# Optimization experiments

Hardware: AMD Instinct MI355X
Metric: run time of the kernel (lower is better)

The kernel has to match this reference:

```python
import jax, jax.numpy as jnp
import numpy as np

NUM_HEADS = 4
KEY_DIMS = 32  # c // num_heads


def rel_to_abs(x):
    # x: [B, N, W, 2W-1] relative logits -> [B, N, W, W] absolute logits
    b, n, w, _ = x.shape
    x = jnp.pad(x, ((0, 0), (0, 0), (0, 0), (0, 1)))           # [b,n,w,2w]
    x = x.reshape(b, n, w * 2 * w)
    x = jnp.pad(x, ((0, 0), (0, 0), (0, w - 1)))
    x = x.reshape(b, n, w + 1, 2 * w - 1)
    return x[:, :, :w, w - 1:]


def rel_logits_1d(q, rel_k):
    # q: [B, heads, X, Y, d], rel_k: [2Y-1, d] -> [B, heads, X, X, Y, Y]
    b, nh, xx, yy, d = q.shape
    rl = jnp.einsum('bhxyd,md->bhxym', q, rel_k)               # [b,h,x,y,2y-1]
    rl = rel_to_abs(rl.reshape(b, nh * xx, yy, 2 * yy - 1))    # [b,h*x,y,y]
    rl = rl.reshape(b, nh, xx, 1, yy, yy)
    return jnp.broadcast_to(rl, (b, nh, xx, xx, yy, yy))


def relative_position_bias(pos_q, pos_emb_h, pos_emb_w):
    # pos_q: [B, heads, H, W, d] -> bias [B, heads, H, W, H, W]
    rw = rel_logits_1d(pos_q, pos_emb_w)                        # [b,h,H,H,W,W]
    rw = rw.transpose(0, 1, 2, 4, 3, 5)                         # [b,h,H,W,H,W]
    rh = rel_logits_1d(pos_q.transpose(0, 1, 3, 2, 4), pos_emb_h)  # [b,h,W,W,H,H]
    rh = rh.transpose(0, 1, 4, 2, 5, 3)                         # [b,h,H,W,H,W]
    return rw + rh


def setup_inputs() -> dict:
    key = jax.random.key(0)
    k1, k2, k3, k4 = jax.random.split(key, 4)
    B, H, W, C = 2, 64, 64, 128
    qk_dims = NUM_HEADS * KEY_DIMS  # 128
    out_channels = C
    x = jax.random.normal(k1, (B, H, W, C), dtype=jnp.float32)
    w_qkv = jax.random.normal(k2, (C, 2 * qk_dims + out_channels), dtype=jnp.float32) * 0.05
    pos_emb_h = jax.random.normal(k3, (2 * H - 1, KEY_DIMS), dtype=jnp.float32) * 0.05
    pos_emb_w = jax.random.normal(k4, (2 * W - 1, KEY_DIMS), dtype=jnp.float32) * 0.05
    return {'x': x, 'w_qkv': w_qkv, 'pos_emb_h': pos_emb_h, 'pos_emb_w': pos_emb_w}


def reference(x, w_qkv, pos_emb_h, pos_emb_w):
    B, H, W, C = x.shape
    nh, kd = NUM_HEADS, KEY_DIMS
    qk_dims = nh * kd
    oc = C
    scale = 1.0 / float(kd) ** 0.5

    qkv = jnp.einsum('bhwc,cd->bhwd', x, w_qkv)                 # 1x1 conv, no bias
    q, k, v = jnp.split(qkv, [qk_dims, 2 * qk_dims], axis=-1)
    L = H * W
    q = q.reshape(B, L, nh, kd).transpose(0, 2, 1, 3)           # [B,nh,L,kd]
    k = k.reshape(B, L, nh, kd).transpose(0, 2, 1, 3)           # [B,nh,L,kd]
    v = v.reshape(B, L, nh, oc // nh).transpose(0, 2, 1, 3)     # [B,nh,L,dv]

    pos_q = q.reshape(B, nh, H, W, kd)
    pos = relative_position_bias(pos_q, pos_emb_h, pos_emb_w).reshape(B, nh, L, L)

    scores = jnp.einsum('bnqd,bnkd->bnqk', q, k) * scale + pos  # [B,nh,L,L]
    attn = jax.nn.softmax(scores, axis=-1)
    out = jnp.einsum('bnqk,bnkd->bnqd', attn, v)                # [B,nh,L,dv]
    out = out.transpose(0, 2, 1, 3).reshape(B, H, W, oc)
    return out
```

## Files before the change

### kernel.cpp

```cpp
#include <hip/hip_runtime.h>
#include <hip/hip_bf16.h>
#include <math.h>

#define B_  2
#define NH  4
#define HH  64
#define WW  64
#define KD  32
#define L_  4096
#define BN_ 8
#define LOG2E 1.4426950408889634f
#define KSCALE (0.17677669529663687f * 1.4426950408889634f)
#define FIXED_M 10.0f

typedef float    f32x4  __attribute__((ext_vector_type(4), may_alias));
typedef _Float16 half8  __attribute__((ext_vector_type(8), may_alias));
typedef _Float16 half4  __attribute__((ext_vector_type(4), may_alias));
typedef __fp16   fp16x2 __attribute__((ext_vector_type(2)));
typedef unsigned uint4v __attribute__((ext_vector_type(4)));

__device__ __forceinline__ float fexp2(float x) {
#if __has_builtin(__builtin_amdgcn_exp2f)
    return __builtin_amdgcn_exp2f(x);
#else
    return __expf(x * 0.69314718056f);
#endif
}

__device__ __forceinline__ unsigned pack2u(float a, float b) {
    fp16x2 t = __builtin_amdgcn_cvt_pkrtz(a, b);
    union { fp16x2 i; unsigned o; } u;
    u.i = t;
    return u.o;
}

__global__ __launch_bounds__(256) void qkv_gemm(const float* __restrict__ x,
                                                const float* __restrict__ w,
                                                _Float16* __restrict__ q_h,
                                                _Float16* __restrict__ k_h,
                                                _Float16* __restrict__ vt_h) {
    __shared__ __align__(16) char smem[34816];
    _Float16* xs  = (_Float16*)smem;
    _Float16* wsT = (_Float16*)(smem + 17408);

    const int mt = blockIdx.x % 128;
    const int nt = blockIdx.x / 128;
    const int m0 = mt * 64, n0 = nt * 64;
    const int tid = threadIdx.x;
    const int wv = tid >> 6, lane = tid & 63;
    const int l16 = lane & 15, quad = lane >> 4;

    #pragma unroll
    for (int i = 0; i < 8; i++) {
        const int idx = i * 256 + tid;
        const int row = idx >> 5, c4 = (idx & 31) * 4;
        const float4 v = *(const float4*)&x[(size_t)(m0 + row) * 128 + c4];
        half4 h;
        h[0] = (_Float16)v.x; h[1] = (_Float16)v.y;
        h[2] = (_Float16)v.z; h[3] = (_Float16)v.w;
        *(half4*)&xs[row * 136 + c4] = h;
    }
    #pragma unroll
    for (int i = 0; i < 8; i++) {
        const int idx = i * 256 + tid;
        const int k = idx >> 4, c4 = (idx & 15) * 4;
        const float4 v = *(const float4*)&w[(size_t)k * 384 + n0 + c4];
        wsT[(c4 + 0) * 136 + k] = (_Float16)v.x;
        wsT[(c4 + 1) * 136 + k] = (_Float16)v.y;
        wsT[(c4 + 2) * 136 + k] = (_Float16)v.z;
        wsT[(c4 + 3) * 136 + k] = (_Float16)v.w;
    }
    __syncthreads();

    f32x4 acc[4] = {{0.f,0.f,0.f,0.f},{0.f,0.f,0.f,0.f},
                    {0.f,0.f,0.f,0.f},{0.f,0.f,0.f,0.f}};
    half8 af[4];
    #pragma unroll
    for (int kc = 0; kc < 4; kc++)
        af[kc] = *(const half8*)&xs[(wv * 16 + l16) * 136 + kc * 32 + quad * 8];
    #pragma unroll
    for (int ns = 0; ns < 4; ns++)
        #pragma unroll
        for (int kc = 0; kc < 4; kc++) {
            const half8 bf = *(const half8*)&wsT[(ns * 16 + l16) * 136 + kc * 32 + quad * 8];
            acc[ns] = __builtin_amdgcn_mfma_f32_16x16x32_f16(af[kc], bf, acc[ns], 0, 0, 0);
        }

    const int which = n0 >> 7;
    const int nc = n0 & 127;
    const int b = m0 >> 12;
    if (which < 2) {
        _Float16* dst = (which == 0) ? q_h : k_h;
        const float mult = (which == 1) ? KSCALE : 1.0f;
        #pragma unroll
        for (int ns = 0; ns < 4; ns++) {
            const int col = nc + ns * 16 + l16;
            const int bn = b * NH + (col >> 5);
            const int d = col & 31;
            #pragma unroll
            for (int r = 0; r < 4; r++) {
                const int l = (m0 & 4095) + wv * 16 + quad * 4 + r;
                dst[((size_t)bn * L_ + l) * 32 + d] = (_Float16)(acc[ns][r] * mult);
            }
        }
    } else {
        __syncthreads();
        float* img = (float*)smem;
        #pragma unroll
        for (int ns = 0; ns < 4; ns++) {
            const int chan = ns * 16 + l16;
            const int h = chan >> 5, d = chan & 31;
            #pragma unroll
            for (int r = 0; r < 4; r++) {
                const int p = wv * 16 + quad * 4 + r;
                const int y = p >> 5, p32 = p & 31;
                const int q4 = (p32 >> 2) & 3;
                const int j = ((p32 >> 4) & 1) * 4 + (p32 & 3);
                const int fidx = h * 2048 + (y * 2 + (d >> 4)) * 512
                               + (q4 * 16 + (d & 15)) * 8 + j;
                img[fidx + (fidx >> 4)] = acc[ns][r];
            }
        }
        __syncthreads();
        const int ktg = (m0 & 4095) >> 6;
        #pragma unroll
        for (int h = 0; h < 2; h++) {
            const int head = (nc >> 5) + h;
            const int bn = b * NH + head;
            const int fbase = h * 2048 + tid * 8;
            const int sbase = fbase + (fbase >> 4);
            half8 o;
            #pragma unroll
            for (int e = 0; e < 8; e++) o[e] = (_Float16)img[sbase + e];
            *(half8*)(vt_h + (size_t)bn * 131072 + ktg * 2048 + tid * 8) = o;
        }
    }
}

__global__ __launch_bounds__(512, 4) void attn_mfma(
    const _Float16* __restrict__ q_h,
    const _Float16* __restrict__ k_h,
    const _Float16* __restrict__ vt_h,
    const float* __restrict__ emb_h,
    const float* __restrict__ emb_w,
    float* __restrict__ out)
{
    __shared__ __align__(16) char smem[33792];

    const int bi   = blockIdx.x;
    const int bn   = bi & 7;
    const int w1   = bi >> 3;
    const int tid  = threadIdx.x;
    const int wv   = tid >> 6;
    const int qwv  = wv & 3;
    const int kh   = wv >> 2;
    const int lane = tid & 63;
    const int l16  = lane & 15;
    const int quad = lane >> 4;
    const int q0   = qwv * 16;

    float* Rl = (float*)smem;

    const half8 aq = *(const half8*)(q_h +
        (((size_t)bn * L_ + (q0 + l16) * 64 + w1) * 32 + quad * 8));

    const _Float16* Kbase = k_h  + (size_t)bn * L_ * 32;
    const _Float16* Vtile = vt_h + (size_t)bn * 131072;
    const int lo = lane * 8;
    const int kt0 = kh * 32;
    const int phase = ((wv & 3) << 3) | ((wv >> 2) << 2);

    int kt = kt0 + phase;
    half8 kf[4];
    #pragma unroll
    for (int sub = 0; sub < 4; sub++)
        kf[sub] = *(const half8*)(Kbase + (size_t)(kt * 64 + sub * 16 + l16) * 32 + quad * 8);

    f32x4 qwT[4];
    #pragma unroll
    for (int sub = 0; sub < 4; sub++) {
        const float* ew = emb_w + (size_t)(sub * 16 + l16 - w1 + 63) * 32 + quad * 8;
        const float4 e0 = *(const float4*)ew;
        const float4 e1 = *(const float4*)(ew + 4);
        union { uint4v u; half8 h; } ua;
        ua.u[0] = pack2u(e0.x * LOG2E, e0.y * LOG2E);
        ua.u[1] = pack2u(e0.z * LOG2E, e0.w * LOG2E);
        ua.u[2] = pack2u(e1.x * LOG2E, e1.y * LOG2E);
        ua.u[3] = pack2u(e1.z * LOG2E, e1.w * LOG2E);
        f32x4 z = {-FIXED_M, -FIXED_M, -FIXED_M, -FIXED_M};
        qwT[sub] = __builtin_amdgcn_mfma_f32_16x16x32_f16(ua.h, aq, z, 0, 0, 0);
    }

    #pragma unroll
    for (int ji = 0; ji < 4; ji++) {
        const int jt = kh * 4 + ji;
        int j = jt * 16 + l16; if (j > 126) j = 126;
        const float* eh = emb_h + (size_t)j * 32 + quad * 8;
        const float4 e0 = *(const float4*)eh;
        const float4 e1 = *(const float4*)(eh + 4);
        union { uint4v u; half8 h; } ub;
        ub.u[0] = pack2u(e0.x * LOG2E, e0.y * LOG2E);
        ub.u[1] = pack2u(e0.z * LOG2E, e0.w * LOG2E);
        ub.u[2] = pack2u(e1.x * LOG2E, e1.y * LOG2E);
        ub.u[3] = pack2u(e1.z * LOG2E, e1.w * LOG2E);
        f32x4 z = {0.f, 0.f, 0.f, 0.f};
        const f32x4 C = __builtin_amdgcn_mfma_f32_16x16x32_f16(aq, ub.h, z, 0, 0, 0);
        #pragma unroll
        for (int r = 0; r < 4; r++)
            Rl[(q0 + quad * 4 + r) * 132 + jt * 16 + l16] = C[r];
    }
    __syncthreads();

    f32x4 O0 = {0.f, 0.f, 0.f, 0.f}, O1 = {0.f, 0.f, 0.f, 0.f};
    float l0 = 0.f, l1 = 0.f;
    const float* qh_ptr = Rl + (q0 + l16) * 132 + 63 - (q0 + l16);
#if __has_builtin(__builtin_amdgcn_fdot2)
    fp16x2 onep;
    { union { unsigned u; fp16x2 h; } uo; uo.u = pack2u(1.0f, 1.0f); onep = uo.h; }
#endif

    #pragma unroll 4
    for (int i = 0; i < 32; i++) {
        const _Float16* tb = Vtile + kt * 2048;
        const half8 va00 = *(const half8*)(tb + lo);
        const half8 va10 = *(const half8*)(tb + 512 + lo);
        const half8 va01 = *(const half8*)(tb + 1024 + lo);
        const half8 va11 = *(const half8*)(tb + 1536 + lo);

        const f32x4 S0 = __builtin_amdgcn_mfma_f32_16x16x32_f16(kf[0], aq, qwT[0], 0, 0, 0);
        const f32x4 S1 = __builtin_amdgcn_mfma_f32_16x16x32_f16(kf[1], aq, qwT[1], 0, 0, 0);
        const f32x4 S2 = __builtin_amdgcn_mfma_f32_16x16x32_f16(kf[2], aq, qwT[2], 0, 0, 0);
        const f32x4 S3 = __builtin_amdgcn_mfma_f32_16x16x32_f16(kf[3], aq, qwT[3], 0, 0, 0);

        const float qh_cur = qh_ptr[kt];

        const int ktn = kt0 + (((kt - kt0) + 1) & 31);
        #pragma unroll
        for (int sub = 0; sub < 4; sub++)
            kf[sub] = *(const half8*)(Kbase + (size_t)(ktn * 64 + sub * 16 + l16) * 32 + quad * 8);

        union { uint4v u; half8 h; } pb0, pb1;
        {
            const float a0 = fexp2(S0[0] + qh_cur), a1 = fexp2(S0[1] + qh_cur);
            const float a2 = fexp2(S0[2] + qh_cur), a3 = fexp2(S0[3] + qh_cur);
            const float b0 = fexp2(S1[0] + qh_cur), b1 = fexp2(S1[1] + qh_cur);
            const float b2 = fexp2(S1[2] + qh_cur), b3 = fexp2(S1[3] + qh_cur);
            pb0.u[0] = pack2u(a0, a1); pb0.u[1] = pack2u(a2, a3);
            pb0.u[2] = pack2u(b0, b1); pb0.u[3] = pack2u(b2, b3);
#if __has_builtin(__builtin_amdgcn_fdot2)
            union { unsigned u; fp16x2 h; } c0, c1, c2, c3;
            c0.u = pb0.u[0]; c1.u = pb0.u[1]; c2.u = pb0.u[2]; c3.u = pb0.u[3];
            l0 = __builtin_amdgcn_fdot2(c0.h, onep, l0, false);
            l0 = __builtin_amdgcn_fdot2(c1.h, onep, l0, false);
            l0 = __builtin_amdgcn_fdot2(c2.h, onep, l0, false);
            l0 = __builtin_amdgcn_fdot2(c3.h, onep, l0, false);
#else
            l0 += ((a0 + a1) + (a2 + a3)) + ((b0 + b1) + (b2 + b3));
#endif
        }
        {
            const float a0 = fexp2(S2[0] + qh_cur), a1 = fexp2(S2[1] + qh_cur);
            const float a2 = fexp2(S2[2] + qh_cur), a3 = fexp2(S2[3] + qh_cur);
            const float b0 = fexp2(S3[0] + qh_cur), b1 = fexp2(S3[1] + qh_cur);
            const float b2 = fexp2(S3[2] + qh_cur), b3 = fexp2(S3[3] + qh_cur);
            pb1.u[0] = pack2u(a0, a1); pb1.u[1] = pack2u(a2, a3);
            pb1.u[2] = pack2u(b0, b1); pb1.u[3] = pack2u(b2, b3);
#if __has_builtin(__builtin_amdgcn_fdot2)
            union { unsigned u; fp16x2 h; } c0, c1, c2, c3;
            c0.u = pb1.u[0]; c1.u = pb1.u[1]; c2.u = pb1.u[2]; c3.u = pb1.u[3];
            l1 = __builtin_amdgcn_fdot2(c0.h, onep, l1, false);
            l1 = __builtin_amdgcn_fdot2(c1.h, onep, l1, false);
            l1 = __builtin_amdgcn_fdot2(c2.h, onep, l1, false);
            l1 = __builtin_amdgcn_fdot2(c3.h, onep, l1, false);
#else
            l1 += ((a0 + a1) + (a2 + a3)) + ((b0 + b1) + (b2 + b3));
#endif
        }

        O0 = __builtin_amdgcn_mfma_f32_16x16x32_f16(va00, pb0.h, O0, 0, 0, 0);
        O0 = __builtin_amdgcn_mfma_f32_16x16x32_f16(va01, pb1.h, O0, 0, 0, 0);
        O1 = __builtin_amdgcn_mfma_f32_16x16x32_f16(va10, pb0.h, O1, 0, 0, 0);
        O1 = __builtin_amdgcn_mfma_f32_16x16x32_f16(va11, pb1.h, O1, 0, 0, 0);

        kt = ktn;
    }

    float l = l0 + l1;
    l += __shfl_xor(l, 16);
    l += __shfl_xor(l, 32);

    __syncthreads();
    float (*mO)[32][17] = (float(*)[32][17])smem;
    float* mL = (float*)(smem + 17408);
    #pragma unroll
    for (int r = 0; r < 4; r++) {
        mO[wv][quad * 4 + r][l16]      = O0[r];
        mO[wv][16 + quad * 4 + r][l16] = O1[r];
    }
    if (quad == 0) mL[wv * 16 + l16] = l;
    __syncthreads();

    const int q  = tid >> 3;
    const int dg = tid & 7;
    const int qg = q >> 4, ql = q & 15;
    const float denom = mL[qg * 16 + ql] + mL[(qg + 4) * 16 + ql];
    const float inv = 1.0f / denom;
    float4 o;
    o.x = (mO[qg][dg * 4 + 0][ql] + mO[qg + 4][dg * 4 + 0][ql]) * inv;
    o.y = (mO[qg][dg * 4 + 1][ql] + mO[qg + 4][dg * 4 + 1][ql]) * inv;
    o.z = (mO[qg][dg * 4 + 2][ql] + mO[qg + 4][dg * 4 + 2][ql]) * inv;
    o.w = (mO[qg][dg * 4 + 3][ql] + mO[qg + 4][dg * 4 + 3][ql]) * inv;
    const int head = bn & 3, bb = bn >> 2;
    *(float4*)&out[(((size_t)bb * 64 + q) * 64 + w1) * 128 + head * 32 + dg * 4] = o;
}

extern "C" void kernel_launch(void* const* d_in, const int* in_sizes, int n_in,
                              void* d_out, int out_size, void* d_ws, size_t ws_size,
                              hipStream_t stream) {
    const float* x     = (const float*)d_in[0];
    const float* w_qkv = (const float*)d_in[1];
    const float* emb_h = (const float*)d_in[2];
    const float* emb_w = (const float*)d_in[3];
    float* out = (float*)d_out;

    _Float16* q_h  = (_Float16*)d_ws;
    _Float16* k_h  = q_h + (size_t)BN_ * L_ * KD;
    _Float16* vt_h = k_h + (size_t)BN_ * L_ * KD;

    qkv_gemm<<<768, 256, 0, stream>>>(x, w_qkv, q_h, k_h, vt_h);
    attn_mfma<<<512, 512, 0, stream>>>(q_h, k_h, vt_h, emb_h, emb_w, out);
}
```

Baseline: 122.9 us.

## Prepack QKV weights into MFMA fragment layout and halve GEMM shared memory

Adds a small pre-kernel that converts the weight matrix to fp16 once, folds in the K scale, and lays it out directly in MFMA B-fragment order. The GEMM then loads its weight fragments straight into registers instead of doing a transposed shared-memory staging pass. The V transpose now goes through shared memory one head at a time so the buffer can shrink to 17 KB, at the cost of extra barriers. The attention kernel's per-wave key-tile phase offset is also changed. Together these aim to cut shared-memory traffic and raise occupancy in the projection GEMM, in exchange for an extra launch.

```diff
diff --git a/kernel.cpp b/kernel.cpp
--- a/kernel.cpp
+++ b/kernel.cpp
@@ -34,14 +34,30 @@
     return u.o;
 }
 
+__global__ __launch_bounds__(64) void pack_w(const float* __restrict__ w,
+                                             _Float16* __restrict__ wpk) {
+    const int bi = blockIdx.x;
+    const int kc = bi & 3;
+    const int ns = (bi >> 2) & 3;
+    const int nt = bi >> 4;
+    const int lane = threadIdx.x;
+    const int l16 = lane & 15, quad = lane >> 4;
+    const float mult = (nt == 2 || nt == 3) ? KSCALE : 1.0f;
+    const int col = nt * 64 + ns * 16 + l16;
+    half8 o;
+    #pragma unroll
+    for (int j = 0; j < 8; j++)
+        o[j] = (_Float16)(w[(size_t)(kc * 32 + quad * 8 + j) * 384 + col] * mult);
+    *(half8*)(wpk + ((size_t)bi * 64 + lane) * 8) = o;
+}
+
 __global__ __launch_bounds__(256) void qkv_gemm(const float* __restrict__ x,
-                                                const float* __restrict__ w,
-                                                _Float16* __restrict__ q_h,
-                                                _Float16* __restrict__ k_h,
-                                                _Float16* __restrict__ vt_h) {
-    __shared__ __align__(16) char smem[34816];
-    _Float16* xs  = (_Float16*)smem;
-    _Float16* wsT = (_Float16*)(smem + 17408);
+                                               const _Float16* __restrict__ wpk,
+                                               _Float16* __restrict__ q_h,
+                                               _Float16* __restrict__ k_h,
+                                               _Float16* __restrict__ vt_h) {
+    __shared__ __align__(16) char smem[17408];
+    _Float16* xs = (_Float16*)smem;
 
     const int mt = blockIdx.x % 128;
     const int nt = blockIdx.x / 128;
@@ -60,16 +76,15 @@
         h[2] = (_Float16)v.z; h[3] = (_Float16)v.w;
         *(half4*)&xs[row * 136 + c4] = h;
     }
-    #pragma unroll
-    for (int i = 0; i < 8; i++) {
-        const int idx = i * 256 + tid;
-        const int k = idx >> 4, c4 = (idx & 15) * 4;
-        const float4 v = *(const float4*)&w[(size_t)k * 384 + n0 + c4];
-        wsT[(c4 + 0) * 136 + k] = (_Float16)v.x;
-        wsT[(c4 + 1) * 136 + k] = (_Float16)v.y;
-        wsT[(c4 + 2) * 136 + k] = (_Float16)v.z;
-        wsT[(c4 + 3) * 136 + k] = (_Float16)v.w;
-    }
+
+    half8 bfr[4][4];
+    #pragma unroll
+    for (int ns = 0; ns < 4; ns++)
+        #pragma unroll
+        for (int kc = 0; kc < 4; kc++)
+            bfr[ns][kc] = *(const half8*)(wpk +
+                ((size_t)(((nt * 4 + ns) * 4 + kc) * 64) + lane) * 8);
+
     __syncthreads();
 
     f32x4 acc[4] = {{0.f,0.f,0.f,0.f},{0.f,0.f,0.f,0.f},
@@ -81,17 +96,15 @@
     #pragma unroll
     for (int ns = 0; ns < 4; ns++)
         #pragma unroll
-        for (int kc = 0; kc < 4; kc++) {
-            const half8 bf = *(const half8*)&wsT[(ns * 16 + l16) * 136 + kc * 32 + quad * 8];
-            acc[ns] = __builtin_amdgcn_mfma_f32_16x16x32_f16(af[kc], bf, acc[ns], 0, 0, 0);
-        }
+        for (int kc = 0; kc < 4; kc++)
+            acc[ns] = __builtin_amdgcn_mfma_f32_16x16x32_f16(af[kc], bfr[ns][kc],
+                                                             acc[ns], 0, 0, 0);
 
     const int which = n0 >> 7;
     const int nc = n0 & 127;
     const int b = m0 >> 12;
     if (which < 2) {
         _Float16* dst = (which == 0) ? q_h : k_h;
-        const float mult = (which == 1) ? KSCALE : 1.0f;
         #pragma unroll
         for (int ns = 0; ns < 4; ns++) {
             const int col = nc + ns * 16 + l16;
@@ -100,7 +113,7 @@
             #pragma unroll
             for (int r = 0; r < 4; r++) {
                 const int l = (m0 & 4095) + wv * 16 + quad * 4 + r;
-                dst[((size_t)bn * L_ + l) * 32 + d] = (_Float16)(acc[ns][r] * mult);
+                dst[((size_t)bn * L_ + l) * 32 + d] = (_Float16)acc[ns][r];
             }
         }
     } else {
@@ -118,17 +131,41 @@
                 const int j = ((p32 >> 4) & 1) * 4 + (p32 & 3);
                 const int fidx = h * 2048 + (y * 2 + (d >> 4)) * 512
                                + (q4 * 16 + (d & 15)) * 8 + j;
-                img[fidx + (fidx >> 4)] = acc[ns][r];
+                if (fidx < 2048) img[fidx + (fidx >> 4)] = acc[ns][r];
             }
         }
         __syncthreads();
         const int ktg = (m0 & 4095) >> 6;
-        #pragma unroll
-        for (int h = 0; h < 2; h++) {
-            const int head = (nc >> 5) + h;
+        {
+            const int head = (nc >> 5);
             const int bn = b * NH + head;
-            const int fbase = h * 2048 + tid * 8;
-            const int sbase = fbase + (fbase >> 4);
+            const int sbase = tid * 8 + (tid >> 1);
+            half8 o;
+            #pragma unroll
+            for (int e = 0; e < 8; e++) o[e] = (_Float16)img[sbase + e];
+            *(half8*)(vt_h + (size_t)bn * 131072 + ktg * 2048 + tid * 8) = o;
+        }
+        __syncthreads();
+        #pragma unroll
+        for (int ns = 0; ns < 4; ns++) {
+            const int chan = ns * 16 + l16;
+            const int h = chan >> 5, d = chan & 31;
+            #pragma unroll
+            for (int r = 0; r < 4; r++) {
+                const int p = wv * 16 + quad * 4 + r;
+                const int y = p >> 5, p32 = p & 31;
+                const int q4 = (p32 >> 2) & 3;
+                const int j = ((p32 >> 4) & 1) * 4 + (p32 & 3);
+                const int fidx = h * 2048 + (y * 2 + (d >> 4)) * 512
+                               + (q4 * 16 + (d & 15)) * 8 + j;
+                if (fidx >= 2048) { const int f2 = fidx - 2048; img[f2 + (f2 >> 4)] = acc[ns][r]; }
+            }
+        }
+        __syncthreads();
+        {
+            const int head = (nc >> 5) + 1;
+            const int bn = b * NH + head;
+            const int sbase = tid * 8 + (tid >> 1);
             half8 o;
             #pragma unroll
             for (int e = 0; e < 8; e++) o[e] = (_Float16)img[sbase + e];
@@ -168,7 +205,7 @@
     const _Float16* Vtile = vt_h + (size_t)bn * 131072;
     const int lo = lane * 8;
     const int kt0 = kh * 32;
-    const int phase = ((wv & 3) << 3) | ((wv >> 2) << 2);
+    const int phase = wv & 3;
 
     int kt = kt0 + phase;
     half8 kf[4];
@@ -326,7 +363,9 @@
     _Float16* q_h  = (_Float16*)d_ws;
     _Float16* k_h  = q_h + (size_t)BN_ * L_ * KD;
     _Float16* vt_h = k_h + (size_t)BN_ * L_ * KD;
-
-    qkv_gemm<<<768, 256, 0, stream>>>(x, w_qkv, q_h, k_h, vt_h);
+    _Float16* wpk  = vt_h + (size_t)BN_ * L_ * KD;
+
+    pack_w<<<96, 64, 0, stream>>>(w_qkv, wpk);
+    qkv_gemm<<<768, 256, 0, stream>>>(x, wpk, q_h, k_h, vt_h);
     attn_mfma<<<512, 512, 0, stream>>>(q_h, k_h, vt_h, emb_h, emb_w, out);
 }
```

After: 123.8 us. About the same (+0.7%).

## Fuse QKV GEMM and attention into one kernel with grid-wide atomic barrier

Applied to the files above, without the earlier changes.

Merges the QKV projection and attention kernels into one persistent launch of 512 blocks of 512 threads. Each block first runs one or two GEMM tiles, then all blocks meet at a software grid barrier built from a global atomic counter and a flag before doing attention. This removes the second kernel launch and its inter-kernel gap, but adds a memset launch and a spin barrier, and it relies on all 512 blocks being co-resident. The K-tile starting phase per wave is also simplified.

```diff
diff --git a/kernel.cpp b/kernel.cpp
--- a/kernel.cpp
+++ b/kernel.cpp
@@ -34,284 +34,296 @@
     return u.o;
 }
 
-__global__ __launch_bounds__(256) void qkv_gemm(const float* __restrict__ x,
-                                                const float* __restrict__ w,
-                                                _Float16* __restrict__ q_h,
-                                                _Float16* __restrict__ k_h,
-                                                _Float16* __restrict__ vt_h) {
+__global__ __launch_bounds__(512) void fused(
+    const float* __restrict__ x,
+    const float* __restrict__ w,
+    const float* __restrict__ emb_h,
+    const float* __restrict__ emb_w,
+    _Float16* __restrict__ q_h,
+    _Float16* __restrict__ k_h,
+    _Float16* __restrict__ vt_h,
+    unsigned* __restrict__ bar,
+    float* __restrict__ out)
+{
     __shared__ __align__(16) char smem[34816];
-    _Float16* xs  = (_Float16*)smem;
-    _Float16* wsT = (_Float16*)(smem + 17408);
-
-    const int mt = blockIdx.x % 128;
-    const int nt = blockIdx.x / 128;
-    const int m0 = mt * 64, n0 = nt * 64;
     const int tid = threadIdx.x;
-    const int wv = tid >> 6, lane = tid & 63;
-    const int l16 = lane & 15, quad = lane >> 4;
-
-    #pragma unroll
-    for (int i = 0; i < 8; i++) {
-        const int idx = i * 256 + tid;
-        const int row = idx >> 5, c4 = (idx & 31) * 4;
-        const float4 v = *(const float4*)&x[(size_t)(m0 + row) * 128 + c4];
-        half4 h;
-        h[0] = (_Float16)v.x; h[1] = (_Float16)v.y;
-        h[2] = (_Float16)v.z; h[3] = (_Float16)v.w;
-        *(half4*)&xs[row * 136 + c4] = h;
+
+    for (int t = blockIdx.x; t < 768; t += 512) {
+        _Float16* xs  = (_Float16*)smem;
+        _Float16* wsT = (_Float16*)(smem + 17408);
+        const int mt = t % 128, nt = t / 128;
+        const int m0 = mt * 64, n0 = nt * 64;
+        const int wv8 = tid >> 6, lane = tid & 63;
+        const int l16 = lane & 15, quad = lane >> 4;
+        const int rw = wv8 & 3;
+        const int ch = wv8 >> 2;
+
+        #pragma unroll
+        for (int i = 0; i < 4; i++) {
+            const int idx = i * 512 + tid;
+            const int row = idx >> 5, c4 = (idx & 31) * 4;
+            const float4 v = *(const float4*)&x[(size_t)(m0 + row) * 128 + c4];
+            half4 h;
+            h[0] = (_Float16)v.x; h[1] = (_Float16)v.y;
+            h[2] = (_Float16)v.z; h[3] = (_Float16)v.w;
+            *(half4*)&xs[row * 136 + c4] = h;
+        }
+        #pragma unroll
+        for (int i = 0; i < 4; i++) {
+            const int idx = i * 512 + tid;
+            const int k = idx >> 4, c4 = (idx & 15) * 4;
+            const float4 v = *(const float4*)&w[(size_t)k * 384 + n0 + c4];
+            wsT[(c4 + 0) * 136 + k] = (_Float16)v.x;
+            wsT[(c4 + 1) * 136 + k] = (_Float16)v.y;
+            wsT[(c4 + 2) * 136 + k] = (_Float16)v.z;
+            wsT[(c4 + 3) * 136 + k] = (_Float16)v.w;
+        }
+        __syncthreads();
+
+        f32x4 acc[2] = {{0.f,0.f,0.f,0.f},{0.f,0.f,0.f,0.f}};
+        half8 af[4];
+        #pragma unroll
+        for (int kc = 0; kc < 4; kc++)
+            af[kc] = *(const half8*)&xs[(rw * 16 + l16) * 136 + kc * 32 + quad * 8];
+        #pragma unroll
+        for (int i = 0; i < 2; i++) {
+            const int ns = ch * 2 + i;
+            #pragma unroll
+            for (int kc = 0; kc < 4; kc++) {
+                const half8 bf = *(const half8*)&wsT[(ns * 16 + l16) * 136 + kc * 32 + quad * 8];
+                acc[i] = __builtin_amdgcn_mfma_f32_16x16x32_f16(af[kc], bf, acc[i], 0, 0, 0);
+            }
+        }
+
+        const int which = n0 >> 7;
+        const int nc = n0 & 127;
+        const int b = m0 >> 12;
+        if (which < 2) {
+            _Float16* dst = (which == 0) ? q_h : k_h;
+            const float mult = (which == 1) ? KSCALE : 1.0f;
+            #pragma unroll
+            for (int i = 0; i < 2; i++) {
+                const int col = nc + (ch * 2 + i) * 16 + l16;
+                const int bn = b * NH + (col >> 5);
+                const int d = col & 31;
+                #pragma unroll
+                for (int r = 0; r < 4; r++) {
+                    const int l = (m0 & 4095) + rw * 16 + quad * 4 + r;
+                    dst[((size_t)bn * L_ + l) * 32 + d] = (_Float16)(acc[i][r] * mult);
+                }
+            }
+            __syncthreads();
+        } else {
+            __syncthreads();
+            float* img = (float*)smem;
+            #pragma unroll
+            for (int i = 0; i < 2; i++) {
+                const int chan = (ch * 2 + i) * 16 + l16;
+                const int h = chan >> 5, d = chan & 31;
+                #pragma unroll
+                for (int r = 0; r < 4; r++) {
+                    const int p = rw * 16 + quad * 4 + r;
+                    const int y = p >> 5, p32 = p & 31;
+                    const int q4 = (p32 >> 2) & 3;
+                    const int j = ((p32 >> 4) & 1) * 4 + (p32 & 3);
+                    const int fidx = h * 2048 + (y * 2 + (d >> 4)) * 512
+                                   + (q4 * 16 + (d & 15)) * 8 + j;
+                    img[fidx + (fidx >> 4)] = acc[i][r];
+                }
+            }
+            __syncthreads();
+            const int ktg = (m0 & 4095) >> 6;
+            const int fbase = tid * 8;
+            const int head = (nc >> 5) + (fbase >> 11);
+            const int bnv = b * NH + head;
+            const int sbase = fbase + (fbase >> 4);
+            half8 o;
+            #pragma unroll
+            for (int e = 0; e < 8; e++) o[e] = (_Float16)img[sbase + e];
+            *(half8*)(vt_h + (size_t)bnv * 131072 + ktg * 2048 + (fbase & 2047)) = o;
+            __syncthreads();
+        }
     }
-    #pragma unroll
-    for (int i = 0; i < 8; i++) {
-        const int idx = i * 256 + tid;
-        const int k = idx >> 4, c4 = (idx & 15) * 4;
-        const float4 v = *(const float4*)&w[(size_t)k * 384 + n0 + c4];
-        wsT[(c4 + 0) * 136 + k] = (_Float16)v.x;
-        wsT[(c4 + 1) * 136 + k] = (_Float16)v.y;
-        wsT[(c4 + 2) * 136 + k] = (_Float16)v.z;
-        wsT[(c4 + 3) * 136 + k] = (_Float16)v.w;
+
+    if (tid == 0) {
+        const unsigned arrived =
+            __hip_atomic_fetch_add(bar, 1u, __ATOMIC_ACQ_REL, __HIP_MEMORY_SCOPE_AGENT);
+        if (arrived == (unsigned)(gridDim.x - 1)) {
+            __hip_atomic_store(bar + 1, 1u, __ATOMIC_RELEASE, __HIP_MEMORY_SCOPE_AGENT);
+        } else {
+            while (__hip_atomic_load(bar + 1, __ATOMIC_ACQUIRE,
+                                     __HIP_MEMORY_SCOPE_AGENT) == 0u)
+                __builtin_amdgcn_s_sleep(8);
+        }
     }
     __syncthreads();
 
-    f32x4 acc[4] = {{0.f,0.f,0.f,0.f},{0.f,0.f,0.f,0.f},
-                    {0.f,0.f,0.f,0.f},{0.f,0.f,0.f,0.f}};
-    half8 af[4];
-    #pragma unroll
-    for (int kc = 0; kc < 4; kc++)
-        af[kc] = *(const half8*)&xs[(wv * 16 + l16) * 136 + kc * 32 + quad * 8];
-    #pragma unroll
-    for (int ns = 0; ns < 4; ns++)
-        #pragma unroll
-        for (int kc = 0; kc < 4; kc++) {
-            const half8 bf = *(const half8*)&wsT[(ns * 16 + l16) * 136 + kc * 32 + quad * 8];
-            acc[ns] = __builtin_amdgcn_mfma_f32_16x16x32_f16(af[kc], bf, acc[ns], 0, 0, 0);
-        }
-
-    const int which = n0 >> 7;
-    const int nc = n0 & 127;
-    const int b = m0 >> 12;
-    if (which < 2) {
-        _Float16* dst = (which == 0) ? q_h : k_h;
-        const float mult = (which == 1) ? KSCALE : 1.0f;
-        #pragma unroll
-        for (int ns = 0; ns < 4; ns++) {
-            const int col = nc + ns * 16 + l16;
-            const int bn = b * NH + (col >> 5);
-            const int d = col & 31;
-            #pragma unroll
-            for (int r = 0; r < 4; r++) {
-                const int l = (m0 & 4095) + wv * 16 + quad * 4 + r;
-                dst[((size_t)bn * L_ + l) * 32 + d] = (_Float16)(acc[ns][r] * mult);
-            }
-        }
-    } else {
+    {
+        const int bi   = blockIdx.x;
+        const int bn   = bi & 7;
+        const int w1   = bi >> 3;
+        const int wv   = tid >> 6;
+        const int qwv  = wv & 3;
+        const int kh   = wv >> 2;
+        const int lane = tid & 63;
+        const int l16  = lane & 15;
+        const int quad = lane >> 4;
+        const int q0   = qwv * 16;
+
+        float* Rl = (float*)smem;
+
+        const half8 aq = *(const half8*)(q_h +
+            (((size_t)bn * L_ + (q0 + l16) * 64 + w1) * 32 + quad * 8));
+
+        const _Float16* Kbase = k_h  + (size_t)bn * L_ * 32;
+        const _Float16* Vtile = vt_h + (size_t)bn * 131072;
+        const int lo = lane * 8;
+        const int kt0 = kh * 32;
+        const int phase = wv & 3;
+
+        int kt = kt0 + phase;
+        half8 kf[4];
+        #pragma unroll
+        for (int sub = 0; sub < 4; sub++)
+            kf[sub] = *(const half8*)(Kbase + (size_t)(kt * 64 + sub * 16 + l16) * 32 + quad * 8);
+
+        f32x4 qwT[4];
+        #pragma unroll
+        for (int sub = 0; sub < 4; sub++) {
+            const float* ew = emb_w + (size_t)(sub * 16 + l16 - w1 + 63) * 32 + quad * 8;
+            const float4 e0 = *(const float4*)ew;
+            const float4 e1 = *(const float4*)(ew + 4);
+            union { uint4v u; half8 h; } ua;
+            ua.u[0] = pack2u(e0.x * LOG2E, e0.y * LOG2E);
+            ua.u[1] = pack2u(e0.z * LOG2E, e0.w * LOG2E);
+            ua.u[2] = pack2u(e1.x * LOG2E, e1.y * LOG2E);
+            ua.u[3] = pack2u(e1.z * LOG2E, e1.w * LOG2E);
+            f32x4 z = {-FIXED_M, -FIXED_M, -FIXED_M, -FIXED_M};
+            qwT[sub] = __builtin_amdgcn_mfma_f32_16x16x32_f16(ua.h, aq, z, 0, 0, 0);
+        }
+
+        #pragma unroll
+        for (int ji = 0; ji < 4; ji++) {
+            const int jt = kh * 4 + ji;
+            int j = jt * 16 + l16; if (j > 126) j = 126;
+            const float* eh = emb_h + (size_t)j * 32 + quad * 8;
+            const float4 e0 = *(const float4*)eh;
+            const float4 e1 = *(const float4*)(eh + 4);
+            union { uint4v u; half8 h; } ub;
+            ub.u[0] = pack2u(e0.x * LOG2E, e0.y * LOG2E);
+            ub.u[1] = pack2u(e0.z * LOG2E, e0.w * LOG2E);
+            ub.u[2] = pack2u(e1.x * LOG2E, e1.y * LOG2E);
+            ub.u[3] = pack2u(e1.z * LOG2E, e1.w * LOG2E);
+            f32x4 z = {0.f, 0.f, 0.f, 0.f};
+            const f32x4 C = __builtin_amdgcn_mfma_f32_16x16x32_f16(aq, ub.h, z, 0, 0, 0);
+            #pragma unroll
+            for (int r = 0; r < 4; r++)
+                Rl[(q0 + quad * 4 + r) * 132 + jt * 16 + l16] = C[r];
+        }
         __syncthreads();
-        float* img = (float*)smem;
-        #pragma unroll
-        for (int ns = 0; ns < 4; ns++) {
-            const int chan = ns * 16 + l16;
-            const int h = chan >> 5, d = chan & 31;
-            #pragma unroll
-            for (int r = 0; r < 4; r++) {
-                const int p = wv * 16 + quad * 4 + r;
-                const int y = p >> 5, p32 = p & 31;
-                const int q4 = (p32 >> 2) & 3;
-                const int j = ((p32 >> 4) & 1) * 4 + (p32 & 3);
-                const int fidx = h * 2048 + (y * 2 + (d >> 4)) * 512
-                               + (q4 * 16 + (d & 15)) * 8 + j;
-                img[fidx + (fidx >> 4)] = acc[ns][r];
-            }
-        }
+
+        f32x4 O0 = {0.f, 0.f, 0.f, 0.f}, O1 = {0.f, 0.f, 0.f, 0.f};
+        float l0 = 0.f, l1 = 0.f;
+        const float* qh_ptr = Rl + (q0 + l16) * 132 + 63 - (q0 + l16);
+#if __has_builtin(__builtin_amdgcn_fdot2)
+        fp16x2 onep;
+        { union { unsigned u; fp16x2 h; } uo; uo.u = pack2u(1.0f, 1.0f); onep = uo.h; }
+#endif
+
+        #pragma unroll 4
+        for (int i = 0; i < 32; i++) {
+            const _Float16* tb = Vtile + kt * 2048;
+            const half8 va00 = *(const half8*)(tb + lo);
+            const half8 va10 = *(const half8*)(tb + 512 + lo);
+            const half8 va01 = *(const half8*)(tb + 1024 + lo);
+            const half8 va11 = *(const half8*)(tb + 1536 + lo);
+
+            const f32x4 S0 = __builtin_amdgcn_mfma_f32_16x16x32_f16(kf[0], aq, qwT[0], 0, 0, 0);
+            const f32x4 S1 = __builtin_amdgcn_mfma_f32_16x16x32_f16(kf[1], aq, qwT[1], 0, 0, 0);
+            const f32x4 S2 = __builtin_amdgcn_mfma_f32_16x16x32_f16(kf[2], aq, qwT[2], 0, 0, 0);
+            const f32x4 S3 = __builtin_amdgcn_mfma_f32_16x16x32_f16(kf[3], aq, qwT[3], 0, 0, 0);
+
+            const float qh_cur = qh_ptr[kt];
+
+            const int ktn = kt0 + (((kt - kt0) + 1) & 31);
+            #pragma unroll
+            for (int sub = 0; sub < 4; sub++)
+                kf[sub] = *(const half8*)(Kbase + (size_t)(ktn * 64 + sub * 16 + l16) * 32 + quad * 8);
+
+            union { uint4v u; half8 h; } pb0, pb1;
+            {
+                const float a0 = fexp2(S0[0] + qh_cur), a1 = fexp2(S0[1] + qh_cur);
+                const float a2 = fexp2(S0[2] + qh_cur), a3 = fexp2(S0[3] + qh_cur);
+                const float b0 = fexp2(S1[0] + qh_cur), b1 = fexp2(S1[1] + qh_cur);
+                const float b2 = fexp2(S1[2] + qh_cur), b3 = fexp2(S1[3] + qh_cur);
+                pb0.u[0] = pack2u(a0, a1); pb0.u[1] = pack2u(a2, a3);
+                pb0.u[2] = pack2u(b0, b1); pb0.u[3] = pack2u(b2, b3);
+#if __has_builtin(__builtin_amdgcn_fdot2)
+                union { unsigned u; fp16x2 h; } c0, c1, c2, c3;
+                c0.u = pb0.u[0]; c1.u = pb0.u[1]; c2.u = pb0.u[2]; c3.u = pb0.u[3];
+                l0 = __builtin_amdgcn_fdot2(c0.h, onep, l0, false);
+                l0 = __builtin_amdgcn_fdot2(c1.h, onep, l0, false);
+                l0 = __builtin_amdgcn_fdot2(c2.h, onep, l0, false);
+                l0 = __builtin_amdgcn_fdot2(c3.h, onep, l0, false);
+#else
+                l0 += ((a0 + a1) + (a2 + a3)) + ((b0 + b1) + (b2 + b3));
+#endif
+            }
+            {
+                const float a0 = fexp2(S2[0] + qh_cur), a1 = fexp2(S2[1] + qh_cur);
+                const float a2 = fexp2(S2[2] + qh_cur), a3 = fexp2(S2[3] + qh_cur);
+                const float b0 = fexp2(S3[0] + qh_cur), b1 = fexp2(S3[1] + qh_cur);
+                const float b2 = fexp2(S3[2] + qh_cur), b3 = fexp2(S3[3] + qh_cur);
+                pb1.u[0] = pack2u(a0, a1); pb1.u[1] = pack2u(a2, a3);
+                pb1.u[2] = pack2u(b0, b1); pb1.u[3] = pack2u(b2, b3);
+#if __has_builtin(__builtin_amdgcn_fdot2)
+                union { unsigned u; fp16x2 h; } c0, c1, c2, c3;
+                c0.u = pb1.u[0]; c1.u = pb1.u[1]; c2.u = pb1.u[2]; c3.u = pb1.u[3];
+                l1 = __builtin_amdgcn_fdot2(c0.h, onep, l1, false);
+                l1 = __builtin_amdgcn_fdot2(c1.h, onep, l1, false);
+                l1 = __builtin_amdgcn_fdot2(c2.h, onep, l1, false);
+                l1 = __builtin_amdgcn_fdot2(c3.h, onep, l1, false);
+#else
+                l1 += ((a0 + a1) + (a2 + a3)) + ((b0 + b1) + (b2 + b3));
+#endif
+            }
+
+            O0 = __builtin_amdgcn_mfma_f32_16x16x32_f16(va00, pb0.h, O0, 0, 0, 0);
+            O0 = __builtin_amdgcn_mfma_f32_16x16x32_f16(va01, pb1.h, O0, 0, 0, 0);
+            O1 = __builtin_amdgcn_mfma_f32_16x16x32_f16(va10, pb0.h, O1, 0, 0, 0);
+            O1 = __builtin_amdgcn_mfma_f32_16x16x32_f16(va11, pb1.h, O1, 0, 0, 0);
+
+            kt = ktn;
+        }
+
+        float l = l0 + l1;
+        l += __shfl_xor(l, 16);
+        l += __shfl_xor(l, 32);
+
         __syncthreads();
-        const int ktg = (m0 & 4095) >> 6;
-        #pragma unroll
-        for (int h = 0; h < 2; h++) {
-            const int head = (nc >> 5) + h;
-            const int bn = b * NH + head;
-            const int fbase = h * 2048 + tid * 8;
-            const int sbase = fbase + (fbase >> 4);
-            half8 o;
-            #pragma unroll
-            for (int e = 0; e < 8; e++) o[e] = (_Float16)img[sbase + e];
-            *(half8*)(vt_h + (size_t)bn * 131072 + ktg * 2048 + tid * 8) = o;
-        }
+        float (*mO)[32][17] = (float(*)[32][17])smem;
+        float* mL = (float*)(smem + 17408);
+        #pragma unroll
+        for (int r = 0; r < 4; r++) {
+            mO[wv][quad * 4 + r][l16]      = O0[r];
+            mO[wv][16 + quad * 4 + r][l16] = O1[r];
+        }
+        if (quad == 0) mL[wv * 16 + l16] = l;
+        __syncthreads();
+
+        const int q  = tid >> 3;
+        const int dg = tid & 7;
+        const int qg = q >> 4, ql = q & 15;
+        const float denom = mL[qg * 16 + ql] + mL[(qg + 4) * 16 + ql];
+        const float inv = 1.0f / denom;
+        float4 o;
+        o.x = (mO[qg][dg * 4 + 0][ql] + mO[qg + 4][dg * 4 + 0][ql]) * inv;
+        o.y = (mO[qg][dg * 4 + 1][ql] + mO[qg + 4][dg * 4 + 1][ql]) * inv;
+        o.z = (mO[qg][dg * 4 + 2][ql] + mO[qg + 4][dg * 4 + 2][ql]) * inv;
+        o.w = (mO[qg][dg * 4 + 3][ql] + mO[qg + 4][dg * 4 + 3][ql]) * inv;
+        const int head = bn & 3, bb = bn >> 2;
+        *(float4*)&out[(((size_t)bb * 64 + q) * 64 + w1) * 128 + head * 32 + dg * 4] = o;
     }
-}
-
-__global__ __launch_bounds__(512, 4) void attn_mfma(
-    const _Float16* __restrict__ q_h,
-    const _Float16* __restrict__ k_h,
-    const _Float16* __restrict__ vt_h,
-    const float* __restrict__ emb_h,
-    const float* __restrict__ emb_w,
-    float* __restrict__ out)
-{
-    __shared__ __align__(16) char smem[33792];
-
-    const int bi   = blockIdx.x;
-    const int bn   = bi & 7;
-    const int w1   = bi >> 3;
-    const int tid  = threadIdx.x;
-    const int wv   = tid >> 6;
-    const int qwv  = wv & 3;
-    const int kh   = wv >> 2;
-    const int lane = tid & 63;
-    const int l16  = lane & 15;
-    const int quad = lane >> 4;
-    const int q0   = qwv * 16;
-
-    float* Rl = (float*)smem;
-
-    const half8 aq = *(const half8*)(q_h +
-        (((size_t)bn * L_ + (q0 + l16) * 64 + w1) * 32 + quad * 8));
-
-    const _Float16* Kbase = k_h  + (size_t)bn * L_ * 32;
-    const _Float16* Vtile = vt_h + (size_t)bn * 131072;
-    const int lo = lane * 8;
-    const int kt0 = kh * 32;
-    const int phase = ((wv & 3) << 3) | ((wv >> 2) << 2);
-
-    int kt = kt0 + phase;
-    half8 kf[4];
-    #pragma unroll
-    for (int sub = 0; sub < 4; sub++)
-        kf[sub] = *(const half8*)(Kbase + (size_t)(kt * 64 + sub * 16 + l16) * 32 + quad * 8);
-
-    f32x4 qwT[4];
-    #pragma unroll
-    for (int sub = 0; sub < 4; sub++) {
-        const float* ew = emb_w + (size_t)(sub * 16 + l16 - w1 + 63) * 32 + quad * 8;
-        const float4 e0 = *(const float4*)ew;
-        const float4 e1 = *(const float4*)(ew + 4);
-        union { uint4v u; half8 h; } ua;
-        ua.u[0] = pack2u(e0.x * LOG2E, e0.y * LOG2E);
-        ua.u[1] = pack2u(e0.z * LOG2E, e0.w * LOG2E);
-        ua.u[2] = pack2u(e1.x * LOG2E, e1.y * LOG2E);
-        ua.u[3] = pack2u(e1.z * LOG2E, e1.w * LOG2E);
-        f32x4 z = {-FIXED_M, -FIXED_M, -FIXED_M, -FIXED_M};
-        qwT[sub] = __builtin_amdgcn_mfma_f32_16x16x32_f16(ua.h, aq, z, 0, 0, 0);
-    }
-
-    #pragma unroll
-    for (int ji = 0; ji < 4; ji++) {
-        const int jt = kh * 4 + ji;
-        int j = jt * 16 + l16; if (j > 126) j = 126;
-        const float* eh = emb_h + (size_t)j * 32 + quad * 8;
-        const float4 e0 = *(const float4*)eh;
-        const float4 e1 = *(const float4*)(eh + 4);
-        union { uint4v u; half8 h; } ub;
-        ub.u[0] = pack2u(e0.x * LOG2E, e0.y * LOG2E);
-        ub.u[1] = pack2u(e0.z * LOG2E, e0.w * LOG2E);
-        ub.u[2] = pack2u(e1.x * LOG2E, e1.y * LOG2E);
-        ub.u[3] = pack2u(e1.z * LOG2E, e1.w * LOG2E);
-        f32x4 z = {0.f, 0.f, 0.f, 0.f};
-        const f32x4 C = __builtin_amdgcn_mfma_f32_16x16x32_f16(aq, ub.h, z, 0, 0, 0);
-        #pragma unroll
-        for (int r = 0; r < 4; r++)
-            Rl[(q0 + quad * 4 + r) * 132 + jt * 16 + l16] = C[r];
-    }
-    __syncthreads();
-
-    f32x4 O0 = {0.f, 0.f, 0.f, 0.f}, O1 = {0.f, 0.f, 0.f, 0.f};
-    float l0 = 0.f, l1 = 0.f;
-    const float* qh_ptr = Rl + (q0 + l16) * 132 + 63 - (q0 + l16);
-#if __has_builtin(__builtin_amdgcn_fdot2)
-    fp16x2 onep;
-    { union { unsigned u; fp16x2 h; } uo; uo.u = pack2u(1.0f, 1.0f); onep = uo.h; }
-#endif
-
-    #pragma unroll 4
-    for (int i = 0; i < 32; i++) {
-        const _Float16* tb = Vtile + kt * 2048;
-        const half8 va00 = *(const half8*)(tb + lo);
-        const half8 va10 = *(const half8*)(tb + 512 + lo);
-        const half8 va01 = *(const half8*)(tb + 1024 + lo);
-        const half8 va11 = *(const half8*)(tb + 1536 + lo);
-
-        const f32x4 S0 = __builtin_amdgcn_mfma_f32_16x16x32_f16(kf[0], aq, qwT[0], 0, 0, 0);
-        const f32x4 S1 = __builtin_amdgcn_mfma_f32_16x16x32_f16(kf[1], aq, qwT[1], 0, 0, 0);
-        const f32x4 S2 = __builtin_amdgcn_mfma_f32_16x16x32_f16(kf[2], aq, qwT[2], 0, 0, 0);
-        const f32x4 S3 = __builtin_amdgcn_mfma_f32_16x16x32_f16(kf[3], aq, qwT[3], 0, 0, 0);
-
-        const float qh_cur = qh_ptr[kt];
-
-        const int ktn = kt0 + (((kt - kt0) + 1) & 31);
-        #pragma unroll
-        for (int sub = 0; sub < 4; sub++)
-            kf[sub] = *(const half8*)(Kbase + (size_t)(ktn * 64 + sub * 16 + l16) * 32 + quad * 8);
-
-        union { uint4v u; half8 h; } pb0, pb1;
-        {
-            const float a0 = fexp2(S0[0] + qh_cur), a1 = fexp2(S0[1] + qh_cur);
-            const float a2 = fexp2(S0[2] + qh_cur), a3 = fexp2(S0[3] + qh_cur);
-            const float b0 = fexp2(S1[0] + qh_cur), b1 = fexp2(S1[1] + qh_cur);
-            const float b2 = fexp2(S1[2] + qh_cur), b3 = fexp2(S1[3] + qh_cur);
-            pb0.u[0] = pack2u(a0, a1); pb0.u[1] = pack2u(a2, a3);
-            pb0.u[2] = pack2u(b0, b1); pb0.u[3] = pack2u(b2, b3);
-#if __has_builtin(__builtin_amdgcn_fdot2)
-            union { unsigned u; fp16x2 h; } c0, c1, c2, c3;
-            c0.u = pb0.u[0]; c1.u = pb0.u[1]; c2.u = pb0.u[2]; c3.u = pb0.u[3];
-            l0 = __builtin_amdgcn_fdot2(c0.h, onep, l0, false);
-            l0 = __builtin_amdgcn_fdot2(c1.h, onep, l0, false);
-            l0 = __builtin_amdgcn_fdot2(c2.h, onep, l0, false);
-            l0 = __builtin_amdgcn_fdot2(c3.h, onep, l0, false);
-#else
-            l0 += ((a0 + a1) + (a2 + a3)) + ((b0 + b1) + (b2 + b3));
-#endif
-        }
-        {
-            const float a0 = fexp2(S2[0] + qh_cur), a1 = fexp2(S2[1] + qh_cur);
-            const float a2 = fexp2(S2[2] + qh_cur), a3 = fexp2(S2[3] + qh_cur);
-            const float b0 = fexp2(S3[0] + qh_cur), b1 = fexp2(S3[1] + qh_cur);
-            const float b2 = fexp2(S3[2] + qh_cur), b3 = fexp2(S3[3] + qh_cur);
-            pb1.u[0] = pack2u(a0, a1); pb1.u[1] = pack2u(a2, a3);
-            pb1.u[2] = pack2u(b0, b1); pb1.u[3] = pack2u(b2, b3);
-#if __has_builtin(__builtin_amdgcn_fdot2)
-            union { unsigned u; fp16x2 h; } c0, c1, c2, c3;
-            c0.u = pb1.u[0]; c1.u = pb1.u[1]; c2.u = pb1.u[2]; c3.u = pb1.u[3];
-            l1 = __builtin_amdgcn_fdot2(c0.h, onep, l1, false);
-            l1 = __builtin_amdgcn_fdot2(c1.h, onep, l1, false);
-            l1 = __builtin_amdgcn_fdot2(c2.h, onep, l1, false);
-            l1 = __builtin_amdgcn_fdot2(c3.h, onep, l1, false);
-#else
-            l1 += ((a0 + a1) + (a2 + a3)) + ((b0 + b1) + (b2 + b3));
-#endif
-        }
-
-        O0 = __builtin_amdgcn_mfma_f32_16x16x32_f16(va00, pb0.h, O0, 0, 0, 0);
-        O0 = __builtin_amdgcn_mfma_f32_16x16x32_f16(va01, pb1.h, O0, 0, 0, 0);
-        O1 = __builtin_amdgcn_mfma_f32_16x16x32_f16(va10, pb0.h, O1, 0, 0, 0);
-        O1 = __builtin_amdgcn_mfma_f32_16x16x32_f16(va11, pb1.h, O1, 0, 0, 0);
-
-        kt = ktn;
-    }
-
-    float l = l0 + l1;
-    l += __shfl_xor(l, 16);
-    l += __shfl_xor(l, 32);
-
-    __syncthreads();
-    float (*mO)[32][17] = (float(*)[32][17])smem;
-    float* mL = (float*)(smem + 17408);
-    #pragma unroll
-    for (int r = 0; r < 4; r++) {
-        mO[wv][quad * 4 + r][l16]      = O0[r];
-        mO[wv][16 + quad * 4 + r][l16] = O1[r];
-    }
-    if (quad == 0) mL[wv * 16 + l16] = l;
-    __syncthreads();
-
-    const int q  = tid >> 3;
-    const int dg = tid & 7;
-    const int qg = q >> 4, ql = q & 15;
-    const float denom = mL[qg * 16 + ql] + mL[(qg + 4) * 16 + ql];
-    const float inv = 1.0f / denom;
-    float4 o;
-    o.x = (mO[qg][dg * 4 + 0][ql] + mO[qg + 4][dg * 4 + 0][ql]) * inv;
-    o.y = (mO[qg][dg * 4 + 1][ql] + mO[qg + 4][dg * 4 + 1][ql]) * inv;
-    o.z = (mO[qg][dg * 4 + 2][ql] + mO[qg + 4][dg * 4 + 2][ql]) * inv;
-    o.w = (mO[qg][dg * 4 + 3][ql] + mO[qg + 4][dg * 4 + 3][ql]) * inv;
-    const int head = bn & 3, bb = bn >> 2;
-    *(float4*)&out[(((size_t)bb * 64 + q) * 64 + w1) * 128 + head * 32 + dg * 4] = o;
 }
 
 extern "C" void kernel_launch(void* const* d_in, const int* in_sizes, int n_in,
@@ -326,7 +338,9 @@
     _Float16* q_h  = (_Float16*)d_ws;
     _Float16* k_h  = q_h + (size_t)BN_ * L_ * KD;
     _Float16* vt_h = k_h + (size_t)BN_ * L_ * KD;
-
-    qkv_gemm<<<768, 256, 0, stream>>>(x, w_qkv, q_h, k_h, vt_h);
-    attn_mfma<<<512, 512, 0, stream>>>(q_h, k_h, vt_h, emb_h, emb_w, out);
+    unsigned* bar  = (unsigned*)(vt_h + (size_t)BN_ * L_ * KD);
+
+    hipMemsetAsync(bar, 0, 2 * sizeof(unsigned), stream);
+    fused<<<512, 512, 0, stream>>>(x, w_qkv, emb_h, emb_w,
+                                   q_h, k_h, vt_h, bar, out);
 }
```

Result: slower. 165.2 us (+34.5%).
